# Performance work log

Measured on AMD Instinct MI355X. Metric: run time of the kernel, lower is better.

The kernel has to match this reference:

```python
import jax, jax.numpy as jnp
import numpy as np

B, N = 32, 512
N_DIM, N_P, N_K = 128, 3, 2
F0_DIM = N_DIM * N_P            # 384
CAT_DIM = N_DIM * (N_K + 1) * N_P  # 1152


def setup_inputs() -> dict:
    key = jax.random.key(0)
    ks = jax.random.split(key, 12)
    s = 0.05
    return {
        "loc": jax.random.uniform(ks[0], (B, N, 2), dtype=jnp.float32),
        "deadline": jax.random.uniform(ks[1], (B, N), dtype=jnp.float32),
        "workload": jax.random.uniform(ks[2], (B, N), dtype=jnp.float32),
        "depot": jax.random.uniform(ks[3], (B, 1, 2), dtype=jnp.float32),
        "W_init": jax.random.normal(ks[4], (3, F0_DIM), dtype=jnp.float32) * s,
        "b_init": jnp.zeros((F0_DIM,), jnp.float32),
        "W_dep": jax.random.normal(ks[5], (2, N_DIM), dtype=jnp.float32) * s,
        "b_dep": jnp.zeros((N_DIM,), jnp.float32),
        "W_g1": jax.random.normal(ks[6], (CAT_DIM, N_DIM), dtype=jnp.float32) * s,
        "b_g1": jnp.zeros((N_DIM,), jnp.float32),
        "W_g2": jax.random.normal(ks[7], (CAT_DIM, N_DIM), dtype=jnp.float32) * s,
        "b_g2": jnp.zeros((N_DIM,), jnp.float32),
        "W_g3": jax.random.normal(ks[8], (CAT_DIM, N_DIM), dtype=jnp.float32) * s,
        "b_g3": jnp.zeros((N_DIM,), jnp.float32),
        "gamma": jnp.ones((F0_DIM,), jnp.float32),
        "beta": jnp.zeros((F0_DIM,), jnp.float32),
        "W_F": jax.random.normal(ks[9], (F0_DIM, N_DIM), dtype=jnp.float32) * s,
        "b_F": jnp.zeros((N_DIM,), jnp.float32),
    }


def _forward(loc, deadline, workload, depot, W_init, b_init, W_dep, b_dep,
             W_g1, b_g1, W_g2, b_g2, W_g3, b_g3, gamma, beta, W_F, b_F):
    # X = [loc, deadline/deadline.max()] -> [B,N,3] (workload is concatenated then dropped in original)
    X = jnp.concatenate([loc, (deadline / deadline.max())[..., None]], axis=-1)
    n = X.shape[1]
    # pairwise squared distances [B,N,N]
    d2 = ((X[:, :, None, :] - X[:, None, :, :]) ** 2).sum(-1)
    off = ~jnp.eye(n, dtype=bool)                      # off-diagonal mask
    d2_safe = jnp.where(off, d2, 1.0)
    A = jnp.where(off, 1.0 / jnp.sqrt(d2_safe), 0.0)   # A = 1/dist off-diag, 0 on diag
    A = jnp.where(jnp.isnan(A), 0.0, A)                # A[A!=A]=0
    A = A / A.max()                                    # global max-normalize
    deg = A.sum(-1) - 1.0                              # (A.sum(-1) - 1)
    L = jnp.eye(n, dtype=A.dtype) * deg[:, None, :] - A  # D - A (diag = deg)
    L2 = L @ L

    F0 = X @ W_init + b_init                           # [B,N,384]
    F0_sq = F0 * F0
    F0_cu = F0 * F0_sq

    def prop(F):
        return jnp.concatenate([F, L @ F, L2 @ F], axis=-1)  # [B,N,1152]

    g1 = prop(F0) @ W_g1 + b_g1
    g2 = prop(F0_sq) @ W_g2 + b_g2
    g3 = prop(F0_cu) @ W_g3 + b_g3
    F1 = jnp.concatenate([g1, g2, g3], axis=-1)        # [B,N,384]
    F1 = jax.nn.leaky_relu(F1) + F0

    # BatchNorm1d (training mode): stats over flattened (B*N) samples, biased var
    flat = F1.reshape(-1, F1.shape[-1])
    mu = flat.mean(0)
    var = ((flat - mu) ** 2).mean(0)
    F1 = (F1 - mu) / jnp.sqrt(var + 1e-5) * gamma + beta

    F_final = jax.nn.leaky_relu(F1 @ W_F + b_F)        # [B,N,128]
    dep = depot @ W_dep + b_dep                        # [B,1,128]
    h = jnp.concatenate([dep, F_final], axis=1)        # [B,N+1,128]
    return h, h.mean(axis=1)


def reference(loc, deadline, workload, depot, W_init, b_init, W_dep, b_dep,
              W_g1, b_g1, W_g2, b_g2, W_g3, b_g3, gamma, beta, W_F, b_F):
    return _forward(loc, deadline, workload, depot, W_init, b_init, W_dep, b_dep,
                    W_g1, b_g1, W_g2, b_g2, W_g3, b_g3, gamma, beta, W_F, b_F)
```

## Files before the change

kernel.cpp:

```cpp
#include <hip/hip_runtime.h>

#define LEAKY(x) ((x) > 0.0f ? (x) : 0.01f * (x))

typedef __attribute__((ext_vector_type(8))) short bf16x8;
typedef __attribute__((ext_vector_type(4))) float f32x4;
typedef __attribute__((ext_vector_type(8))) unsigned short u16x8;
typedef __attribute__((ext_vector_type(4))) unsigned short u16x4;

__device__ __forceinline__ unsigned short f2bf(float f) {
    unsigned int u = __float_as_uint(f);
    unsigned int r = (u + 0x7fffu + ((u >> 16) & 1u)) >> 16;
    return (unsigned short)r;
}
__device__ __forceinline__ float bf2f(unsigned short u) {
    return __uint_as_float(((unsigned int)u) << 16);
}

__device__ __forceinline__ void lds_barrier() {
    __builtin_amdgcn_s_waitcnt(0xC07F);
    __builtin_amdgcn_s_barrier();
}


__global__ void k_dmax(const float* __restrict__ deadline, float* __restrict__ dmax) {
    __shared__ float red[256];
    int t = threadIdx.x;
    float m = -1e30f;
    for (int i = t; i < 16384; i += 256) m = fmaxf(m, deadline[i]);
    red[t] = m; __syncthreads();
    for (int s = 128; s > 0; s >>= 1) {
        if (t < s) red[t] = fmaxf(red[t], red[t + s]);
        __syncthreads();
    }
    if (t == 0) *dmax = red[0];
}

__global__ __launch_bounds__(256) void k_rowstats(const float* __restrict__ loc,
                                                  const float* __restrict__ deadline,
                                                  const float* __restrict__ dmaxv,
                                                  float* __restrict__ rowsum, float* __restrict__ pmax) {
    int blk = blockIdx.x;
    int wave = threadIdx.x >> 6, lane = threadIdx.x & 63;
    int bi = blk * 4 + wave;
    int b = bi >> 9, i = bi & 511;
    float invd = 1.0f / (*dmaxv);
    const float* lb = loc + b * 1024;
    const float* db = deadline + b * 512;
    float xi = lb[i * 2], yi = lb[i * 2 + 1], zi = db[i] * invd;
    float lsum = 0.f, lmax = 0.f;
    for (int j = lane; j < 512; j += 64) {
        float d0 = xi - lb[j * 2], d1 = yi - lb[j * 2 + 1], d2 = zi - db[j] * invd;
        float dd = d0 * d0 + d1 * d1 + d2 * d2;
        float r = (j == i) ? 0.f : rsqrtf(dd);
        lsum += r; lmax = fmaxf(lmax, r);
    }
    for (int off = 32; off > 0; off >>= 1) {
        lsum += __shfl_down(lsum, off);
        lmax = fmaxf(lmax, __shfl_down(lmax, off));
    }
    __shared__ float smax[4];
    if (lane == 0) { rowsum[bi] = lsum; smax[wave] = lmax; }
    __syncthreads();
    if (threadIdx.x == 0) pmax[blk] = fmaxf(fmaxf(smax[0], smax[1]), fmaxf(smax[2], smax[3]));
}

__global__ void k_amax(const float* __restrict__ pmax, float* __restrict__ amaxf) {
    __shared__ float red[256];
    int t = threadIdx.x;
    float m = 0.f;
    for (int i = t; i < 4096; i += 256) m = fmaxf(m, pmax[i]);
    red[t] = m; __syncthreads();
    for (int s = 128; s > 0; s >>= 1) {
        if (t < s) red[t] = fmaxf(red[t], red[t + s]);
        __syncthreads();
    }
    if (t == 0) *amaxf = red[0];
}

__global__ void k_buildL(const float* __restrict__ loc, const float* __restrict__ deadline,
                         const float* __restrict__ dmaxv, const float* __restrict__ rowsum,
                         const float* __restrict__ amaxf, unsigned short* __restrict__ Lb) {
    int id = blockIdx.x * 256 + threadIdx.x;
    float inv = 1.0f / (*amaxf);
    float invd = 1.0f / (*dmaxv);
    size_t e = (size_t)id * 4;
    size_t bi = e >> 9;
    int b = (int)(bi >> 9);
    int i = (int)(bi & 511);
    int j0 = (int)(e & 511);
    const float* lb = loc + b * 1024;
    const float* db = deadline + b * 512;
    float xi = lb[i * 2], yi = lb[i * 2 + 1], zi = db[i] * invd;
    float4 l01 = *(const float4*)(lb + j0 * 2);
    float4 l23 = *(const float4*)(lb + j0 * 2 + 4);
    float4 dj = *(const float4*)(db + j0);
    float diag = rowsum[bi] * inv - 1.0f;
    float jx[4] = {l01.x, l01.z, l23.x, l23.z};
    float jy[4] = {l01.y, l01.w, l23.y, l23.w};
    float jz[4] = {dj.x * invd, dj.y * invd, dj.z * invd, dj.w * invd};
    u16x4 o;
#pragma unroll
    for (int j = 0; j < 4; j++) {
        float d0 = xi - jx[j], d1 = yi - jy[j], d2 = zi - jz[j];
        float dd = d0 * d0 + d1 * d1 + d2 * d2;
        float v = (i == j0 + j) ? diag : -rsqrtf(dd) * inv;
        o[j] = f2bf(v);
    }
    *(u16x4*)(Lb + e) = o;
}

__global__ void k_F0powW(const float* __restrict__ loc, const float* __restrict__ deadline,
                         const float* __restrict__ dmaxv,
                         const float* __restrict__ Wi, const float* __restrict__ bi_,
                         const float* __restrict__ Wg1, const float* __restrict__ Wg2,
                         const float* __restrict__ Wg3,
                         unsigned short* __restrict__ P1, unsigned short* __restrict__ P2,
                         unsigned short* __restrict__ P3, unsigned short* __restrict__ WgT) {
    int bid = blockIdx.x;
    if (bid < 6144) {
        int id = bid * 256 + threadIdx.x;
        int row = id / 96, c4 = (id % 96) * 4;
        float x0 = loc[row * 2], x1 = loc[row * 2 + 1], x2 = deadline[row] / (*dmaxv);
        float4 w0 = *(const float4*)(Wi + c4);
        float4 w1 = *(const float4*)(Wi + 384 + c4);
        float4 w2 = *(const float4*)(Wi + 768 + c4);
        float4 bb = *(const float4*)(bi_ + c4);
        float f[4] = {x0 * w0.x + x1 * w1.x + x2 * w2.x + bb.x,
                      x0 * w0.y + x1 * w1.y + x2 * w2.y + bb.y,
                      x0 * w0.z + x1 * w1.z + x2 * w2.z + bb.z,
                      x0 * w0.w + x1 * w1.w + x2 * w2.w + bb.w};
        u16x4 o1, o2, o3;
#pragma unroll
        for (int j = 0; j < 4; j++) {
            o1[j] = f2bf(f[j]); o2[j] = f2bf(f[j] * f[j]); o3[j] = f2bf(f[j] * f[j] * f[j]);
        }
        size_t e = (size_t)row * 384 + c4;
        *(u16x4*)(P1 + e) = o1; *(u16x4*)(P2 + e) = o2; *(u16x4*)(P3 + e) = o3;
    } else {
        int id = (bid - 6144) * 256 + threadIdx.x;
        int combo = id / 49152, rem = id % 49152;
        int n = rem / 384, k = rem % 384;
        int kp = combo / 3, part = combo % 3;
        const float* W = (kp == 0) ? Wg1 : (kp == 1 ? Wg2 : Wg3);
        WgT[id] = f2bf(W[(part * 384 + k) * 128 + n]);
    }
}


__device__ __forceinline__ void pipe128x64(
    const unsigned short* __restrict__ A0, int As0, const unsigned short* __restrict__ B0, int Bs0, int it0,
    const unsigned short* __restrict__ A1, int As1, const unsigned short* __restrict__ B1, int Bs1, int it1,
    unsigned short* AsL, unsigned short* BsL,
    f32x4 (&acc)[4][2], int t)
{
    const int lane = t & 63, wave = t >> 6;
    const int wm = wave >> 1, wn = wave & 1;
    const int quad = lane >> 4, l16 = lane & 15;
    const int ra = t >> 1, ca = (t & 1) * 4;
    const int rb = t >> 2, cb = (t & 3) * 2;
    const unsigned short* Ar0 = A0 + (size_t)ra * As0;
    const unsigned short* Ar1 = A1 ? (A1 + (size_t)ra * As1) : Ar0;
    const unsigned short* Br0 = B0 + (size_t)rb * Bs0;
    const unsigned short* Br1 = B1 ? (B1 + (size_t)rb * Bs1) : Br0;
    const int total = it0 + it1;

    u16x8 paA[4], pbA[2], paB[4], pbB[2];
    auto loadStage = [&](int idx, u16x8 (&pa)[4], u16x8 (&pb)[2]) {
        int sg = (idx >= it0);
        int k0 = (sg ? idx - it0 : idx) * 64;
        const unsigned short* Ar = sg ? Ar1 : Ar0;
        const unsigned short* Br = sg ? Br1 : Br0;
#pragma unroll
        for (int j = 0; j < 4; j++) pa[j] = *(const u16x8*)(Ar + k0 + (ca + j) * 8);
#pragma unroll
        for (int j = 0; j < 2; j++) pb[j] = *(const u16x8*)(Br + k0 + (cb + j) * 8);
    };
    auto writeStage = [&](int bf_, u16x8 (&pa)[4], u16x8 (&pb)[2]) {
#pragma unroll
        for (int j = 0; j < 4; j++)
            *(u16x8*)(AsL + bf_ * 8192 + ra * 64 + (((ca + j) ^ (ra & 7)) * 8)) = pa[j];
#pragma unroll
        for (int j = 0; j < 2; j++)
            *(u16x8*)(BsL + bf_ * 4096 + rb * 64 + (((cb + j) ^ (rb & 7)) * 8)) = pb[j];
    };
    auto mfmaStep = [&](int bf_) {
#pragma unroll
        for (int h = 0; h < 2; h++) {
            bf16x8 af[4], bfr[2];
            int phys = ((h * 4 + quad) ^ (l16 & 7)) * 8;
#pragma unroll
            for (int i = 0; i < 4; i++)
                af[i] = *(const bf16x8*)(AsL + bf_ * 8192 + (wm * 64 + i * 16 + l16) * 64 + phys);
#pragma unroll
            for (int n = 0; n < 2; n++)
                bfr[n] = *(const bf16x8*)(BsL + bf_ * 4096 + (wn * 32 + n * 16 + l16) * 64 + phys);
#pragma unroll
            for (int i = 0; i < 4; i++)
#pragma unroll
                for (int n = 0; n < 2; n++)
                    acc[i][n] = __builtin_amdgcn_mfma_f32_16x16x32_bf16(af[i], bfr[n], acc[i][n], 0, 0, 0);
        }
    };

    loadStage(0, paA, pbA);
    loadStage(1, paB, pbB);
    int buf = 0;
    for (int s = 0; s < total; s += 2) {
        writeStage(buf, paA, pbA);
        lds_barrier();
        if (s + 2 < total) loadStage(s + 2, paA, pbA);
        mfmaStep(buf);
        buf ^= 1;
        writeStage(buf, paB, pbB);
        lds_barrier();
        if (s + 3 < total) loadStage(s + 3, paB, pbB);
        mfmaStep(buf);
        buf ^= 1;
    }
}

__device__ __forceinline__ void pipe64x64(
    const unsigned short* __restrict__ A0, int As0, const unsigned short* __restrict__ B0, int Bs0, int it0,
    unsigned short* AsL, unsigned short* BsL,
    f32x4 (&acc)[2][2], int t)
{
    const int lane = t & 63, wave = t >> 6;
    const int wm = wave >> 1, wn = wave & 1;
    const int quad = lane >> 4, l16 = lane & 15;
    const int rb = t >> 2, cb = (t & 3) * 2;
    const unsigned short* Ar0 = A0 + (size_t)rb * As0;
    const unsigned short* Br0 = B0 + (size_t)rb * Bs0;

    u16x8 paA[2], pbA[2], paB[2], pbB[2];
    auto loadStage = [&](int idx, u16x8 (&pa)[2], u16x8 (&pb)[2]) {
        int k0 = idx * 64;
#pragma unroll
        for (int j = 0; j < 2; j++) { pa[j] = *(const u16x8*)(Ar0 + k0 + (cb + j) * 8);
                                      pb[j] = *(const u16x8*)(Br0 + k0 + (cb + j) * 8); }
    };
    auto writeStage = [&](int bf_, u16x8 (&pa)[2], u16x8 (&pb)[2]) {
#pragma unroll
        for (int j = 0; j < 2; j++) {
            int phys = ((cb + j) ^ (rb & 7)) * 8;
            *(u16x8*)(AsL + bf_ * 4096 + rb * 64 + phys) = pa[j];
            *(u16x8*)(BsL + bf_ * 4096 + rb * 64 + phys) = pb[j];
        }
    };
    auto mfmaStep = [&](int bf_) {
#pragma unroll
        for (int h = 0; h < 2; h++) {
            bf16x8 af[2], bfr[2];
            int phys = ((h * 4 + quad) ^ (l16 & 7)) * 8;
#pragma unroll
            for (int i = 0; i < 2; i++)
                af[i] = *(const bf16x8*)(AsL + bf_ * 4096 + (wm * 32 + i * 16 + l16) * 64 + phys);
#pragma unroll
            for (int n = 0; n < 2; n++)
                bfr[n] = *(const bf16x8*)(BsL + bf_ * 4096 + (wn * 32 + n * 16 + l16) * 64 + phys);
#pragma unroll
            for (int i = 0; i < 2; i++)
#pragma unroll
                for (int n = 0; n < 2; n++)
                    acc[i][n] = __builtin_amdgcn_mfma_f32_16x16x32_bf16(af[i], bfr[n], acc[i][n], 0, 0, 0);
        }
    };

    loadStage(0, paA, pbA);
    loadStage(1, paB, pbB);
    int buf = 0;
    for (int s = 0; s < it0; s += 2) {
        writeStage(buf, paA, pbA);
        lds_barrier();
        if (s + 2 < it0) loadStage(s + 2, paA, pbA);
        mfmaStep(buf);
        buf ^= 1;
        writeStage(buf, paB, pbB);
        lds_barrier();
        if (s + 3 < it0) loadStage(s + 3, paB, pbB);
        mfmaStep(buf);
        buf ^= 1;
    }
}

__device__ __forceinline__ void storeCT_bf16(
    f32x4 (&acc)[4][2], unsigned short* LDSu, int t, unsigned short* __restrict__ dst)
{
    const int wave = t >> 6, lane = t & 63;
    const int wm = wave >> 1, wn = wave & 1;
    const int quad = lane >> 4, l16 = lane & 15;
    __syncthreads();
    unsigned short* Cs = LDSu;
#pragma unroll
    for (int i = 0; i < 4; i++)
#pragma unroll
        for (int n = 0; n < 2; n++)
#pragma unroll
            for (int r = 0; r < 4; r++)
                Cs[(wm * 64 + i * 16 + quad * 4 + r) * 72 + wn * 32 + n * 16 + l16] = f2bf(acc[i][n][r]);
    __syncthreads();
#pragma unroll
    for (int v = 0; v < 4; v++) {
        int chunk = t + v * 256;
        int row = chunk >> 3, c8 = (chunk & 7) * 8;
        u16x8 val = *(u16x8*)(Cs + row * 72 + c8);
        *(u16x8*)(dst + (size_t)row * 512 + c8) = val;
    }
}

__global__ __launch_bounds__(256) void k_ygemmT(
    const unsigned short* __restrict__ WgT,
    const unsigned short* __restrict__ P1, const unsigned short* __restrict__ P2,
    const unsigned short* __restrict__ P3, unsigned short* __restrict__ Y2T)
{
    __shared__ unsigned short LDSu[24576];
    const int t = threadIdx.x;
    const int id = blockIdx.x;
    const int b = id & 31, tt = id >> 5;
    const int kp = tt % 3, nb = tt / 3;
    const unsigned short* P = (kp == 0) ? P1 : (kp == 1 ? P2 : P3);
    f32x4 acc[4][2];
#pragma unroll
    for (int i = 0; i < 4; i++)
#pragma unroll
        for (int n = 0; n < 2; n++) acc[i][n] = (f32x4){0.f, 0.f, 0.f, 0.f};
    pipe128x64(WgT + (size_t)(kp * 3 + 2) * 49152, 384,
               P + ((size_t)b * 512 + nb * 64) * 384, 384, 6,
               nullptr, 0, nullptr, 0, 0, LDSu, LDSu + 16384, acc, t);
    storeCT_bf16(acc, LDSu, t, Y2T + ((size_t)b * 384 + kp * 128) * 512 + nb * 64);
}

__global__ __launch_bounds__(256) void k_lg1T(
    const unsigned short* __restrict__ Lb, const unsigned short* __restrict__ Y2T,
    const unsigned short* __restrict__ WgT,
    const unsigned short* __restrict__ P1, const unsigned short* __restrict__ P2,
    const unsigned short* __restrict__ P3, unsigned short* __restrict__ ZT)
{
    __shared__ unsigned short LDSu[24576];
    const int t = threadIdx.x;
    const int id = blockIdx.x;
    const int b = id & 31, tt = id >> 5;
    const int kp = tt % 3, nb = tt / 3;
    const unsigned short* P = (kp == 0) ? P1 : (kp == 1 ? P2 : P3);
    f32x4 acc[4][2];
#pragma unroll
    for (int i = 0; i < 4; i++)
#pragma unroll
        for (int n = 0; n < 2; n++) acc[i][n] = (f32x4){0.f, 0.f, 0.f, 0.f};
    pipe128x64(Y2T + (size_t)b * 196608 + (size_t)kp * 128 * 512, 512,
               Lb + (size_t)b * 262144 + (size_t)nb * 64 * 512, 512, 8,
               WgT + (size_t)(kp * 3 + 1) * 49152, 384,
               P + ((size_t)b * 512 + nb * 64) * 384, 384, 6, LDSu, LDSu + 16384, acc, t);
    storeCT_bf16(acc, LDSu, t, ZT + ((size_t)b * 384 + kp * 128) * 512 + nb * 64);
}

__global__ __launch_bounds__(256) void k_lg2(
    const unsigned short* __restrict__ Lb, const unsigned short* __restrict__ ZT,
    const unsigned short* __restrict__ WgT,
    const unsigned short* __restrict__ P1, const unsigned short* __restrict__ P2,
    const unsigned short* __restrict__ P3,
    const float* __restrict__ bg1, const float* __restrict__ bg2, const float* __restrict__ bg3,
    unsigned short* __restrict__ F1b, float* __restrict__ bn1, float* __restrict__ bn2)
{
    __shared__ unsigned short LDSu[24576];
    __shared__ float bnS[64], bnQ[64];
    const int t = threadIdx.x;
    const int id = blockIdx.x;
    const int b = id & 31, tt = id >> 5;
    const int gt = tt % 6, mb = tt / 6;
    const int kp = gt >> 1;
    if (t < 64) { bnS[t] = 0.f; bnQ[t] = 0.f; }
    const unsigned short* P = (kp == 0) ? P1 : (kp == 1 ? P2 : P3);
    f32x4 acc[4][2];
#pragma unroll
    for (int i = 0; i < 4; i++)
#pragma unroll
        for (int n = 0; n < 2; n++) acc[i][n] = (f32x4){0.f, 0.f, 0.f, 0.f};
    pipe128x64(Lb + (size_t)b * 262144 + (size_t)mb * 128 * 512, 512,
               ZT + (size_t)b * 196608 + (size_t)gt * 64 * 512, 512, 8,
               P + ((size_t)b * 512 + mb * 128) * 384, 384,
               WgT + (size_t)(kp * 3) * 49152 + (size_t)(gt & 1) * 64 * 384, 384, 6,
               LDSu, LDSu + 16384, acc, t);

    const int wave = t >> 6, lane = t & 63;
    const int wm = wave >> 1, wn = wave & 1;
    const int quad = lane >> 4, l16 = lane & 15;
    __syncthreads();
    float* Cf = (float*)LDSu;
#pragma unroll
    for (int i = 0; i < 4; i++)
#pragma unroll
        for (int n = 0; n < 2; n++)
#pragma unroll
            for (int r = 0; r < 4; r++)
                Cf[(wm * 64 + i * 16 + quad * 4 + r) * 68 + wn * 32 + n * 16 + l16] = acc[i][n][r];
    __syncthreads();

    const float* bg = (kp == 0) ? bg1 : (kp == 1 ? bg2 : bg3);
    float4 bgv = *(const float4*)(bg + (gt & 1) * 64 + (t & 15) * 4);
    float ls1[4] = {0.f, 0.f, 0.f, 0.f}, ls2[4] = {0.f, 0.f, 0.f, 0.f};
#pragma unroll
    for (int v = 0; v < 8; v++) {
        int chunk = t + v * 256;
        int row = chunk >> 4;
        int c4 = (chunk & 15) * 4;
        float4 a = *(float4*)(Cf + row * 68 + c4);
        size_t idx = ((size_t)b * 512 + mb * 128 + row) * 384 + gt * 64 + c4;
        u16x4 p = *(const u16x4*)(P1 + idx);
        float av[4] = {a.x, a.y, a.z, a.w};
        float bv[4] = {bgv.x, bgv.y, bgv.z, bgv.w};
        u16x4 o;
#pragma unroll
        for (int j = 0; j < 4; j++) {
            float c = av[j] + bv[j];
            float vv = LEAKY(c) + bf2f(p[j]);
            o[j] = f2bf(vv);
            ls1[j] += vv; ls2[j] += vv * vv;
        }
        *(u16x4*)(F1b + idx) = o;
    }
#pragma unroll
    for (int j = 0; j < 4; j++) {
        atomicAdd(&bnS[(t & 15) * 4 + j], ls1[j]);
        atomicAdd(&bnQ[(t & 15) * 4 + j], ls2[j]);
    }
    __syncthreads();
    if (t < 64) {
        atomicAdd(&bn1[gt * 64 + t], bnS[t]);
        atomicAdd(&bn2[gt * 64 + t], bnQ[t]);
    }
}

__global__ __launch_bounds__(384) void k_bnprep(
    const float* __restrict__ bn1, const float* __restrict__ bn2,
    const float* __restrict__ gamma, const float* __restrict__ beta,
    const float* __restrict__ WF, const float* __restrict__ bF,
    float* __restrict__ sS, float* __restrict__ beffv)
{
    __shared__ float ttL[384];
    int c = threadIdx.x;
    float mu = bn1[c] * (1.f / 16384.f);
    float var = bn2[c] * (1.f / 16384.f) - mu * mu;
    float sc = gamma[c] / sqrtf(var + 1e-5f);
    sS[c] = sc;
    ttL[c] = beta[c] - mu * sc;
    __syncthreads();
    if (c < 128) {
        float a = bF[c];
        for (int k = 0; k < 384; k++) a += ttL[k] * WF[k * 128 + c];
        beffv[c] = a;
    }
}

__global__ void k_foldDep(const float* __restrict__ WF, const float* __restrict__ sS,
                          const float* __restrict__ depot, const float* __restrict__ Wd,
                          const float* __restrict__ bd,
                          unsigned short* __restrict__ WFsT, float* __restrict__ out) {
    int bid = blockIdx.x, t = threadIdx.x;
    if (bid < 192) {
        int id = bid * 256 + t;
        int n = id / 384, k = id % 384;
        WFsT[id] = f2bf(WF[k * 128 + n] * sS[k]);
    } else {
        int id = (bid - 192) * 256 + t;
        int b = id >> 7, o = id & 127;
        out[(size_t)b * 65664 + o] = depot[b * 2] * Wd[o] + depot[b * 2 + 1] * Wd[128 + o] + bd[o];
    }
}

__global__ __launch_bounds__(256) void k_fgemm(
    const unsigned short* __restrict__ F1b, const unsigned short* __restrict__ WFsT,
    const float* __restrict__ beffv, float* __restrict__ out, float* __restrict__ msum)
{
    __shared__ unsigned short LDSu[16384];
    __shared__ float msS[64];
    const int t = threadIdx.x;
    const int id = blockIdx.x;
    const int b = id & 31, tt = id >> 5;
    const int seg = tt >> 1, nt = tt & 1;
    if (t < 64) msS[t] = 0.f;
    f32x4 acc[2][2];
#pragma unroll
    for (int i = 0; i < 2; i++)
#pragma unroll
        for (int n = 0; n < 2; n++) acc[i][n] = (f32x4){0.f, 0.f, 0.f, 0.f};
    pipe64x64(F1b + ((size_t)b * 512 + seg * 64) * 384, 384,
              WFsT + (size_t)nt * 64 * 384, 384, 6, LDSu, LDSu + 8192, acc, t);

    const int wave = t >> 6, lane = t & 63;
    const int wm = wave >> 1, wn = wave & 1;
    const int quad = lane >> 4, l16 = lane & 15;
    __syncthreads();
    float* Cf = (float*)LDSu;
#pragma unroll
    for (int i = 0; i < 2; i++)
#pragma unroll
        for (int n = 0; n < 2; n++)
#pragma unroll
            for (int r = 0; r < 4; r++)
                Cf[(wm * 32 + i * 16 + quad * 4 + r) * 68 + wn * 32 + n * 16 + l16] = acc[i][n][r];
    __syncthreads();

    float4 be = *(const float4*)(beffv + nt * 64 + (t & 15) * 4);
    float ls[4] = {0.f, 0.f, 0.f, 0.f};
#pragma unroll
    for (int v = 0; v < 4; v++) {
        int chunk = t + v * 256;
        int row = chunk >> 4;
        int c4 = (chunk & 15) * 4;
        float4 a = *(float4*)(Cf + row * 68 + c4);
        float av[4] = {a.x, a.y, a.z, a.w};
        float bv[4] = {be.x, be.y, be.z, be.w};
        float vv0 = LEAKY(av[0] + bv[0]); ls[0] += vv0;
        float vv1 = LEAKY(av[1] + bv[1]); ls[1] += vv1;
        float vv2 = LEAKY(av[2] + bv[2]); ls[2] += vv2;
        float vv3 = LEAKY(av[3] + bv[3]); ls[3] += vv3;
        *(float4*)(out + (size_t)b * 65664 + (size_t)(seg * 64 + row + 1) * 128 + nt * 64 + c4)
            = make_float4(vv0, vv1, vv2, vv3);
    }
#pragma unroll
    for (int j = 0; j < 4; j++) atomicAdd(&msS[(t & 15) * 4 + j], ls[j]);
    __syncthreads();
    if (t < 64) atomicAdd(&msum[b * 128 + nt * 64 + t], msS[t]);
}

__global__ void k_mean(const float* __restrict__ msum, float* __restrict__ out) {
    int id = blockIdx.x * 256 + threadIdx.x;
    int b = id >> 7, o = id & 127;
    float dep = out[(size_t)b * 65664 + o];
    out[2101248 + id] = (msum[id] + dep) * (1.0f / 513.0f);
}


extern "C" void kernel_launch(void* const* d_in, const int* in_sizes, int n_in,
                              void* d_out, int out_size, void* d_ws, size_t ws_size,
                              hipStream_t stream) {
    const float* loc      = (const float*)d_in[0];
    const float* deadline = (const float*)d_in[1];
    const float* depot    = (const float*)d_in[3];
    const float* W_init   = (const float*)d_in[4];
    const float* b_init   = (const float*)d_in[5];
    const float* W_dep    = (const float*)d_in[6];
    const float* b_dep    = (const float*)d_in[7];
    const float* W_g1     = (const float*)d_in[8];
    const float* b_g1     = (const float*)d_in[9];
    const float* W_g2     = (const float*)d_in[10];
    const float* b_g2     = (const float*)d_in[11];
    const float* W_g3     = (const float*)d_in[12];
    const float* b_g3     = (const float*)d_in[13];
    const float* gamma    = (const float*)d_in[14];
    const float* beta     = (const float*)d_in[15];
    const float* W_F      = (const float*)d_in[16];
    const float* b_F      = (const float*)d_in[17];
    float* out = (float*)d_out;
    float* ws  = (float*)d_ws;

    float* dmaxv  = ws + 0;
    float* amaxf  = ws + 4;
    float* bn1    = ws + 8;
    float* bn2    = ws + 392;
    float* msum   = ws + 776;
    float* rowsum = ws + 4872;
    float* pmax   = ws + 21256;
    float* sS     = ws + 25352;
    float* beffv  = ws + 25736;
    unsigned short* Lb   = (unsigned short*)(ws + 25864);
    unsigned short* P1   = (unsigned short*)(ws + 4220168);
    unsigned short* P2   = (unsigned short*)(ws + 7365896);
    unsigned short* P3   = (unsigned short*)(ws + 10511624);
    unsigned short* WgT  = (unsigned short*)(ws + 13657352);
    unsigned short* WFsT = (unsigned short*)(ws + 13878536);
    unsigned short* Y2T  = (unsigned short*)(ws + 13903112);
    unsigned short* ZT   = (unsigned short*)(ws + 17048840);
    unsigned short* F1b  = (unsigned short*)(ws + 20194568);

    hipMemsetAsync(bn1, 0, (384 + 384 + 4096) * sizeof(float), stream);

    k_dmax<<<1, 256, 0, stream>>>(deadline, dmaxv);
    k_rowstats<<<4096, 256, 0, stream>>>(loc, deadline, dmaxv, rowsum, pmax);
    k_amax<<<1, 256, 0, stream>>>(pmax, amaxf);
    k_buildL<<<8192, 256, 0, stream>>>(loc, deadline, dmaxv, rowsum, amaxf, Lb);
    k_F0powW<<<7872, 256, 0, stream>>>(loc, deadline, dmaxv, W_init, b_init,
                                       W_g1, W_g2, W_g3, P1, P2, P3, WgT);

    k_ygemmT<<<768, 256, 0, stream>>>(WgT, P1, P2, P3, Y2T);
    k_lg1T<<<768, 256, 0, stream>>>(Lb, Y2T, WgT, P1, P2, P3, ZT);
    k_lg2<<<768, 256, 0, stream>>>(Lb, ZT, WgT, P1, P2, P3,
                                   b_g1, b_g2, b_g3, F1b, bn1, bn2);

    k_bnprep<<<1, 384, 0, stream>>>(bn1, bn2, gamma, beta, W_F, b_F, sS, beffv);
    k_foldDep<<<208, 256, 0, stream>>>(W_F, sS, depot, W_dep, b_dep, WFsT, out);
    k_fgemm<<<512, 256, 0, stream>>>(F1b, WFsT, beffv, out, msum);
    k_mean<<<16, 256, 0, stream>>>(msum, out);
}
```

Measured before the change: 241.2 us.

## Use 128x128 output tiles for L-propagation GEMMs and regroup block-to-batch mapping

The two Laplacian propagation GEMMs (k_lg1T, k_lg2) switch from 128x64 tiles with K-step 64 to 128x128 tiles with K-step 32, halving their grid to 384 blocks. This doubles per-block data reuse and cuts redundant loads of L and the weight/feature operands. All GEMM kernels also remap block IDs so that eight consecutive blocks cover eight batches of the same tile, which may change L2 locality. The k_lg2 epilogue now applies bias and leaky ReLU before staging results to LDS as bf16, adding an extra rounding step. The larger tile raises accumulator register use and leaves fewer blocks to fill the CUs.

Result: slower. 250.6 us (+3.9%).

```diff
diff --git a/kernel.cpp b/kernel.cpp
--- a/kernel.cpp
+++ b/kernel.cpp
@@ -149,7 +149,6 @@
 
 __device__ __forceinline__ void pipe128x64(
     const unsigned short* __restrict__ A0, int As0, const unsigned short* __restrict__ B0, int Bs0, int it0,
-    const unsigned short* __restrict__ A1, int As1, const unsigned short* __restrict__ B1, int Bs1, int it1,
     unsigned short* AsL, unsigned short* BsL,
     f32x4 (&acc)[4][2], int t)
 {
@@ -159,21 +158,15 @@
     const int ra = t >> 1, ca = (t & 1) * 4;
     const int rb = t >> 2, cb = (t & 3) * 2;
     const unsigned short* Ar0 = A0 + (size_t)ra * As0;
-    const unsigned short* Ar1 = A1 ? (A1 + (size_t)ra * As1) : Ar0;
     const unsigned short* Br0 = B0 + (size_t)rb * Bs0;
-    const unsigned short* Br1 = B1 ? (B1 + (size_t)rb * Bs1) : Br0;
-    const int total = it0 + it1;
 
     u16x8 paA[4], pbA[2], paB[4], pbB[2];
     auto loadStage = [&](int idx, u16x8 (&pa)[4], u16x8 (&pb)[2]) {
-        int sg = (idx >= it0);
-        int k0 = (sg ? idx - it0 : idx) * 64;
-        const unsigned short* Ar = sg ? Ar1 : Ar0;
-        const unsigned short* Br = sg ? Br1 : Br0;
-#pragma unroll
-        for (int j = 0; j < 4; j++) pa[j] = *(const u16x8*)(Ar + k0 + (ca + j) * 8);
-#pragma unroll
-        for (int j = 0; j < 2; j++) pb[j] = *(const u16x8*)(Br + k0 + (cb + j) * 8);
+        int k0 = idx * 64;
+#pragma unroll
+        for (int j = 0; j < 4; j++) pa[j] = *(const u16x8*)(Ar0 + k0 + (ca + j) * 8);
+#pragma unroll
+        for (int j = 0; j < 2; j++) pb[j] = *(const u16x8*)(Br0 + k0 + (cb + j) * 8);
     };
     auto writeStage = [&](int bf_, u16x8 (&pa)[4], u16x8 (&pb)[2]) {
 #pragma unroll
@@ -196,69 +189,6 @@
                 bfr[n] = *(const bf16x8*)(BsL + bf_ * 4096 + (wn * 32 + n * 16 + l16) * 64 + phys);
 #pragma unroll
             for (int i = 0; i < 4; i++)
-#pragma unroll
-                for (int n = 0; n < 2; n++)
-                    acc[i][n] = __builtin_amdgcn_mfma_f32_16x16x32_bf16(af[i], bfr[n], acc[i][n], 0, 0, 0);
-        }
-    };
-
-    loadStage(0, paA, pbA);
-    loadStage(1, paB, pbB);
-    int buf = 0;
-    for (int s = 0; s < total; s += 2) {
-        writeStage(buf, paA, pbA);
-        lds_barrier();
-        if (s + 2 < total) loadStage(s + 2, paA, pbA);
-        mfmaStep(buf);
-        buf ^= 1;
-        writeStage(buf, paB, pbB);
-        lds_barrier();
-        if (s + 3 < total) loadStage(s + 3, paB, pbB);
-        mfmaStep(buf);
-        buf ^= 1;
-    }
-}
-
-__device__ __forceinline__ void pipe64x64(
-    const unsigned short* __restrict__ A0, int As0, const unsigned short* __restrict__ B0, int Bs0, int it0,
-    unsigned short* AsL, unsigned short* BsL,
-    f32x4 (&acc)[2][2], int t)
-{
-    const int lane = t & 63, wave = t >> 6;
-    const int wm = wave >> 1, wn = wave & 1;
-    const int quad = lane >> 4, l16 = lane & 15;
-    const int rb = t >> 2, cb = (t & 3) * 2;
-    const unsigned short* Ar0 = A0 + (size_t)rb * As0;
-    const unsigned short* Br0 = B0 + (size_t)rb * Bs0;
-
-    u16x8 paA[2], pbA[2], paB[2], pbB[2];
-    auto loadStage = [&](int idx, u16x8 (&pa)[2], u16x8 (&pb)[2]) {
-        int k0 = idx * 64;
-#pragma unroll
-        for (int j = 0; j < 2; j++) { pa[j] = *(const u16x8*)(Ar0 + k0 + (cb + j) * 8);
-                                      pb[j] = *(const u16x8*)(Br0 + k0 + (cb + j) * 8); }
-    };
-    auto writeStage = [&](int bf_, u16x8 (&pa)[2], u16x8 (&pb)[2]) {
-#pragma unroll
-        for (int j = 0; j < 2; j++) {
-            int phys = ((cb + j) ^ (rb & 7)) * 8;
-            *(u16x8*)(AsL + bf_ * 4096 + rb * 64 + phys) = pa[j];
-            *(u16x8*)(BsL + bf_ * 4096 + rb * 64 + phys) = pb[j];
-        }
-    };
-    auto mfmaStep = [&](int bf_) {
-#pragma unroll
-        for (int h = 0; h < 2; h++) {
-            bf16x8 af[2], bfr[2];
-            int phys = ((h * 4 + quad) ^ (l16 & 7)) * 8;
-#pragma unroll
-            for (int i = 0; i < 2; i++)
-                af[i] = *(const bf16x8*)(AsL + bf_ * 4096 + (wm * 32 + i * 16 + l16) * 64 + phys);
-#pragma unroll
-            for (int n = 0; n < 2; n++)
-                bfr[n] = *(const bf16x8*)(BsL + bf_ * 4096 + (wn * 32 + n * 16 + l16) * 64 + phys);
-#pragma unroll
-            for (int i = 0; i < 2; i++)
 #pragma unroll
                 for (int n = 0; n < 2; n++)
                     acc[i][n] = __builtin_amdgcn_mfma_f32_16x16x32_bf16(af[i], bfr[n], acc[i][n], 0, 0, 0);
@@ -282,6 +212,136 @@
     }
 }
 
+__device__ __forceinline__ void pipe128x128(
+    const unsigned short* __restrict__ A0, int As0, const unsigned short* __restrict__ B0, int Bs0, int it0,
+    const unsigned short* __restrict__ A1, int As1, const unsigned short* __restrict__ B1, int Bs1, int it1,
+    unsigned short* AsL, unsigned short* BsL,
+    f32x4 (&acc)[4][4], int t)
+{
+    const int lane = t & 63, wave = t >> 6;
+    const int wm = wave >> 1, wn = wave & 1;
+    const int quad = lane >> 4, l16 = lane & 15;
+    const int r_ = t >> 1, c_ = (t & 1) * 2;
+    const unsigned short* ArA = A0 + (size_t)r_ * As0;
+    const unsigned short* ArB = A1 ? (A1 + (size_t)r_ * As1) : ArA;
+    const unsigned short* BrA = B0 + (size_t)r_ * Bs0;
+    const unsigned short* BrB = B1 ? (B1 + (size_t)r_ * Bs1) : BrA;
+    const int total = it0 + it1;
+
+    u16x8 pa0[2], pb0[2], pa1[2], pb1[2];
+    auto loadStage = [&](int idx, u16x8 (&pa)[2], u16x8 (&pb)[2]) {
+        int sg = (idx >= it0);
+        int k0 = (sg ? idx - it0 : idx) * 32;
+        const unsigned short* Ar = sg ? ArB : ArA;
+        const unsigned short* Br = sg ? BrB : BrA;
+#pragma unroll
+        for (int j = 0; j < 2; j++) { pa[j] = *(const u16x8*)(Ar + k0 + (c_ + j) * 8);
+                                      pb[j] = *(const u16x8*)(Br + k0 + (c_ + j) * 8); }
+    };
+    auto writeStage = [&](int bf_, u16x8 (&pa)[2], u16x8 (&pb)[2]) {
+#pragma unroll
+        for (int j = 0; j < 2; j++) {
+            int phys = ((c_ + j) ^ (r_ & 3)) * 8;
+            *(u16x8*)(AsL + bf_ * 4096 + r_ * 32 + phys) = pa[j];
+            *(u16x8*)(BsL + bf_ * 4096 + r_ * 32 + phys) = pb[j];
+        }
+    };
+    auto mfmaStep = [&](int bf_) {
+        bf16x8 af[4], bfr[4];
+        int phys = (quad ^ (l16 & 3)) * 8;
+#pragma unroll
+        for (int i = 0; i < 4; i++)
+            af[i] = *(const bf16x8*)(AsL + bf_ * 4096 + (wm * 64 + i * 16 + l16) * 32 + phys);
+#pragma unroll
+        for (int n = 0; n < 4; n++)
+            bfr[n] = *(const bf16x8*)(BsL + bf_ * 4096 + (wn * 64 + n * 16 + l16) * 32 + phys);
+#pragma unroll
+        for (int i = 0; i < 4; i++)
+#pragma unroll
+            for (int n = 0; n < 4; n++)
+                acc[i][n] = __builtin_amdgcn_mfma_f32_16x16x32_bf16(af[i], bfr[n], acc[i][n], 0, 0, 0);
+    };
+
+    loadStage(0, pa0, pb0);
+    loadStage(1, pa1, pb1);
+    int buf = 0;
+    for (int s = 0; s < total; s += 2) {
+        writeStage(buf, pa0, pb0);
+        lds_barrier();
+        if (s + 2 < total) loadStage(s + 2, pa0, pb0);
+        mfmaStep(buf);
+        buf ^= 1;
+        writeStage(buf, pa1, pb1);
+        lds_barrier();
+        if (s + 3 < total) loadStage(s + 3, pa1, pb1);
+        mfmaStep(buf);
+        buf ^= 1;
+    }
+}
+
+__device__ __forceinline__ void pipe64x64(
+    const unsigned short* __restrict__ A0, int As0, const unsigned short* __restrict__ B0, int Bs0, int it0,
+    unsigned short* AsL, unsigned short* BsL,
+    f32x4 (&acc)[2][2], int t)
+{
+    const int lane = t & 63, wave = t >> 6;
+    const int wm = wave >> 1, wn = wave & 1;
+    const int quad = lane >> 4, l16 = lane & 15;
+    const int rb = t >> 2, cb = (t & 3) * 2;
+    const unsigned short* Ar0 = A0 + (size_t)rb * As0;
+    const unsigned short* Br0 = B0 + (size_t)rb * Bs0;
+
+    u16x8 paA[2], pbA[2], paB[2], pbB[2];
+    auto loadStage = [&](int idx, u16x8 (&pa)[2], u16x8 (&pb)[2]) {
+        int k0 = idx * 64;
+#pragma unroll
+        for (int j = 0; j < 2; j++) { pa[j] = *(const u16x8*)(Ar0 + k0 + (cb + j) * 8);
+                                      pb[j] = *(const u16x8*)(Br0 + k0 + (cb + j) * 8); }
+    };
+    auto writeStage = [&](int bf_, u16x8 (&pa)[2], u16x8 (&pb)[2]) {
+#pragma unroll
+        for (int j = 0; j < 2; j++) {
+            int phys = ((cb + j) ^ (rb & 7)) * 8;
+            *(u16x8*)(AsL + bf_ * 4096 + rb * 64 + phys) = pa[j];
+            *(u16x8*)(BsL + bf_ * 4096 + rb * 64 + phys) = pb[j];
+        }
+    };
+    auto mfmaStep = [&](int bf_) {
+#pragma unroll
+        for (int h = 0; h < 2; h++) {
+            bf16x8 af[2], bfr[2];
+            int phys = ((h * 4 + quad) ^ (l16 & 7)) * 8;
+#pragma unroll
+            for (int i = 0; i < 2; i++)
+                af[i] = *(const bf16x8*)(AsL + bf_ * 4096 + (wm * 32 + i * 16 + l16) * 64 + phys);
+#pragma unroll
+            for (int n = 0; n < 2; n++)
+                bfr[n] = *(const bf16x8*)(BsL + bf_ * 4096 + (wn * 32 + n * 16 + l16) * 64 + phys);
+#pragma unroll
+            for (int i = 0; i < 2; i++)
+#pragma unroll
+                for (int n = 0; n < 2; n++)
+                    acc[i][n] = __builtin_amdgcn_mfma_f32_16x16x32_bf16(af[i], bfr[n], acc[i][n], 0, 0, 0);
+        }
+    };
+
+    loadStage(0, paA, pbA);
+    loadStage(1, paB, pbB);
+    int buf = 0;
+    for (int s = 0; s < it0; s += 2) {
+        writeStage(buf, paA, pbA);
+        lds_barrier();
+        if (s + 2 < it0) loadStage(s + 2, paA, pbA);
+        mfmaStep(buf);
+        buf ^= 1;
+        writeStage(buf, paB, pbB);
+        lds_barrier();
+        if (s + 3 < it0) loadStage(s + 3, paB, pbB);
+        mfmaStep(buf);
+        buf ^= 1;
+    }
+}
+
 __device__ __forceinline__ void storeCT_bf16(
     f32x4 (&acc)[4][2], unsigned short* LDSu, int t, unsigned short* __restrict__ dst)
 {
@@ -289,21 +349,42 @@
     const int wm = wave >> 1, wn = wave & 1;
     const int quad = lane >> 4, l16 = lane & 15;
     __syncthreads();
-    unsigned short* Cs = LDSu;
 #pragma unroll
     for (int i = 0; i < 4; i++)
 #pragma unroll
         for (int n = 0; n < 2; n++)
 #pragma unroll
             for (int r = 0; r < 4; r++)
-                Cs[(wm * 64 + i * 16 + quad * 4 + r) * 72 + wn * 32 + n * 16 + l16] = f2bf(acc[i][n][r]);
+                LDSu[(wm * 64 + i * 16 + quad * 4 + r) * 72 + wn * 32 + n * 16 + l16] = f2bf(acc[i][n][r]);
     __syncthreads();
 #pragma unroll
     for (int v = 0; v < 4; v++) {
         int chunk = t + v * 256;
         int row = chunk >> 3, c8 = (chunk & 7) * 8;
-        u16x8 val = *(u16x8*)(Cs + row * 72 + c8);
-        *(u16x8*)(dst + (size_t)row * 512 + c8) = val;
+        *(u16x8*)(dst + (size_t)row * 512 + c8) = *(u16x8*)(LDSu + row * 72 + c8);
+    }
+}
+
+__device__ __forceinline__ void storeCT128(
+    f32x4 (&acc)[4][4], unsigned short* LDSu, int t, unsigned short* __restrict__ dst)
+{
+    const int wave = t >> 6, lane = t & 63;
+    const int wm = wave >> 1, wn = wave & 1;
+    const int quad = lane >> 4, l16 = lane & 15;
+    __syncthreads();
+#pragma unroll
+    for (int i = 0; i < 4; i++)
+#pragma unroll
+        for (int n = 0; n < 4; n++)
+#pragma unroll
+            for (int r = 0; r < 4; r++)
+                LDSu[(wm * 64 + i * 16 + quad * 4 + r) * 136 + wn * 64 + n * 16 + l16] = f2bf(acc[i][n][r]);
+    __syncthreads();
+#pragma unroll
+    for (int v = 0; v < 8; v++) {
+        int chunk = t + v * 256;
+        int row = chunk >> 4, c8 = (chunk & 15) * 8;
+        *(u16x8*)(dst + (size_t)row * 512 + c8) = *(u16x8*)(LDSu + row * 136 + c8);
     }
 }
 
@@ -315,8 +396,10 @@
     __shared__ unsigned short LDSu[24576];
     const int t = threadIdx.x;
     const int id = blockIdx.x;
-    const int b = id & 31, tt = id >> 5;
-    const int kp = tt % 3, nb = tt / 3;
+    const int hi = id >> 3;
+    const int tile = hi % 24;
+    const int b = (id & 7) + ((hi / 24) << 3);
+    const int kp = tile % 3, nb = tile / 3;
     const unsigned short* P = (kp == 0) ? P1 : (kp == 1 ? P2 : P3);
     f32x4 acc[4][2];
 #pragma unroll
@@ -325,7 +408,7 @@
         for (int n = 0; n < 2; n++) acc[i][n] = (f32x4){0.f, 0.f, 0.f, 0.f};
     pipe128x64(WgT + (size_t)(kp * 3 + 2) * 49152, 384,
                P + ((size_t)b * 512 + nb * 64) * 384, 384, 6,
-               nullptr, 0, nullptr, 0, 0, LDSu, LDSu + 16384, acc, t);
+               LDSu, LDSu + 16384, acc, t);
     storeCT_bf16(acc, LDSu, t, Y2T + ((size_t)b * 384 + kp * 128) * 512 + nb * 64);
 }
 
@@ -335,22 +418,25 @@
     const unsigned short* __restrict__ P1, const unsigned short* __restrict__ P2,
     const unsigned short* __restrict__ P3, unsigned short* __restrict__ ZT)
 {
-    __shared__ unsigned short LDSu[24576];
+    __shared__ unsigned short LDSu[17408];
     const int t = threadIdx.x;
     const int id = blockIdx.x;
-    const int b = id & 31, tt = id >> 5;
-    const int kp = tt % 3, nb = tt / 3;
+    const int hi = id >> 3;
+    const int tile = hi % 12;
+    const int b = (id & 7) + ((hi / 12) << 3);
+    const int kp = tile % 3, nb = tile / 3;
     const unsigned short* P = (kp == 0) ? P1 : (kp == 1 ? P2 : P3);
-    f32x4 acc[4][2];
+    f32x4 acc[4][4];
 #pragma unroll
     for (int i = 0; i < 4; i++)
 #pragma unroll
-        for (int n = 0; n < 2; n++) acc[i][n] = (f32x4){0.f, 0.f, 0.f, 0.f};
-    pipe128x64(Y2T + (size_t)b * 196608 + (size_t)kp * 128 * 512, 512,
-               Lb + (size_t)b * 262144 + (size_t)nb * 64 * 512, 512, 8,
-               WgT + (size_t)(kp * 3 + 1) * 49152, 384,
-               P + ((size_t)b * 512 + nb * 64) * 384, 384, 6, LDSu, LDSu + 16384, acc, t);
-    storeCT_bf16(acc, LDSu, t, ZT + ((size_t)b * 384 + kp * 128) * 512 + nb * 64);
+        for (int n = 0; n < 4; n++) acc[i][n] = (f32x4){0.f, 0.f, 0.f, 0.f};
+    pipe128x128(Y2T + (size_t)b * 196608 + (size_t)kp * 128 * 512, 512,
+                Lb + (size_t)b * 262144 + (size_t)nb * 128 * 512, 512, 16,
+                WgT + (size_t)(kp * 3 + 1) * 49152, 384,
+                P + ((size_t)b * 512 + nb * 128) * 384, 384, 12,
+                LDSu, LDSu + 8192, acc, t);
+    storeCT128(acc, LDSu, t, ZT + ((size_t)b * 384 + kp * 128) * 512 + nb * 128);
 }
 
 __global__ __launch_bounds__(256) void k_lg2(
@@ -361,72 +447,73 @@
     const float* __restrict__ bg1, const float* __restrict__ bg2, const float* __restrict__ bg3,
     unsigned short* __restrict__ F1b, float* __restrict__ bn1, float* __restrict__ bn2)
 {
-    __shared__ unsigned short LDSu[24576];
-    __shared__ float bnS[64], bnQ[64];
+    __shared__ unsigned short LDSu[17408];
+    __shared__ float bnS[128], bnQ[128];
     const int t = threadIdx.x;
     const int id = blockIdx.x;
-    const int b = id & 31, tt = id >> 5;
-    const int gt = tt % 6, mb = tt / 6;
-    const int kp = gt >> 1;
-    if (t < 64) { bnS[t] = 0.f; bnQ[t] = 0.f; }
-    const unsigned short* P = (kp == 0) ? P1 : (kp == 1 ? P2 : P3);
-    f32x4 acc[4][2];
+    const int hi = id >> 3;
+    const int tile = hi % 12;
+    const int b = (id & 7) + ((hi / 12) << 3);
+    const int mb = tile & 3, gt = tile >> 2;
+    if (t < 128) { bnS[t] = 0.f; bnQ[t] = 0.f; }
+    const unsigned short* P = (gt == 0) ? P1 : (gt == 1 ? P2 : P3);
+    f32x4 acc[4][4];
 #pragma unroll
     for (int i = 0; i < 4; i++)
 #pragma unroll
-        for (int n = 0; n < 2; n++) acc[i][n] = (f32x4){0.f, 0.f, 0.f, 0.f};
-    pipe128x64(Lb + (size_t)b * 262144 + (size_t)mb * 128 * 512, 512,
-               ZT + (size_t)b * 196608 + (size_t)gt * 64 * 512, 512, 8,
-               P + ((size_t)b * 512 + mb * 128) * 384, 384,
-               WgT + (size_t)(kp * 3) * 49152 + (size_t)(gt & 1) * 64 * 384, 384, 6,
-               LDSu, LDSu + 16384, acc, t);
+        for (int n = 0; n < 4; n++) acc[i][n] = (f32x4){0.f, 0.f, 0.f, 0.f};
+    pipe128x128(Lb + (size_t)b * 262144 + (size_t)mb * 128 * 512, 512,
+                ZT + (size_t)b * 196608 + (size_t)gt * 128 * 512, 512, 16,
+                P + ((size_t)b * 512 + mb * 128) * 384, 384,
+                WgT + (size_t)(gt * 3) * 49152, 384, 12,
+                LDSu, LDSu + 8192, acc, t);
 
     const int wave = t >> 6, lane = t & 63;
     const int wm = wave >> 1, wn = wave & 1;
     const int quad = lane >> 4, l16 = lane & 15;
-    __syncthreads();
-    float* Cf = (float*)LDSu;
+    const float* bg = (gt == 0) ? bg1 : (gt == 1 ? bg2 : bg3);
+    __syncthreads();
 #pragma unroll
     for (int i = 0; i < 4; i++)
 #pragma unroll
-        for (int n = 0; n < 2; n++)
-#pragma unroll
-            for (int r = 0; r < 4; r++)
-                Cf[(wm * 64 + i * 16 + quad * 4 + r) * 68 + wn * 32 + n * 16 + l16] = acc[i][n][r];
-    __syncthreads();
-
-    const float* bg = (kp == 0) ? bg1 : (kp == 1 ? bg2 : bg3);
-    float4 bgv = *(const float4*)(bg + (gt & 1) * 64 + (t & 15) * 4);
-    float ls1[4] = {0.f, 0.f, 0.f, 0.f}, ls2[4] = {0.f, 0.f, 0.f, 0.f};
+        for (int n = 0; n < 4; n++) {
+            int colL = wn * 64 + n * 16 + l16;
+            float bias = bg[colL];
+#pragma unroll
+            for (int r = 0; r < 4; r++) {
+                float c = acc[i][n][r] + bias;
+                LDSu[(wm * 64 + i * 16 + quad * 4 + r) * 136 + colL] = f2bf(LEAKY(c));
+            }
+        }
+    __syncthreads();
+    float ls1[8] = {0.f,0.f,0.f,0.f,0.f,0.f,0.f,0.f};
+    float ls2[8] = {0.f,0.f,0.f,0.f,0.f,0.f,0.f,0.f};
 #pragma unroll
     for (int v = 0; v < 8; v++) {
         int chunk = t + v * 256;
         int row = chunk >> 4;
-        int c4 = (chunk & 15) * 4;
-        float4 a = *(float4*)(Cf + row * 68 + c4);
-        size_t idx = ((size_t)b * 512 + mb * 128 + row) * 384 + gt * 64 + c4;
-        u16x4 p = *(const u16x4*)(P1 + idx);
-        float av[4] = {a.x, a.y, a.z, a.w};
-        float bv[4] = {bgv.x, bgv.y, bgv.z, bgv.w};
-        u16x4 o;
-#pragma unroll
-        for (int j = 0; j < 4; j++) {
-            float c = av[j] + bv[j];
-            float vv = LEAKY(c) + bf2f(p[j]);
+        int c8 = (chunk & 15) * 8;
+        size_t idx = ((size_t)b * 512 + mb * 128 + row) * 384 + gt * 128 + c8;
+        u16x8 st = *(u16x8*)(LDSu + row * 136 + c8);
+        u16x8 p  = *(const u16x8*)(P1 + idx);
+        u16x8 o;
+#pragma unroll
+        for (int j = 0; j < 8; j++) {
+            float vv = bf2f(st[j]) + bf2f(p[j]);
             o[j] = f2bf(vv);
             ls1[j] += vv; ls2[j] += vv * vv;
         }
-        *(u16x4*)(F1b + idx) = o;
-    }
-#pragma unroll
-    for (int j = 0; j < 4; j++) {
-        atomicAdd(&bnS[(t & 15) * 4 + j], ls1[j]);
-        atomicAdd(&bnQ[(t & 15) * 4 + j], ls2[j]);
-    }
-    __syncthreads();
-    if (t < 64) {
-        atomicAdd(&bn1[gt * 64 + t], bnS[t]);
-        atomicAdd(&bn2[gt * 64 + t], bnQ[t]);
+        *(u16x8*)(F1b + idx) = o;
+    }
+#pragma unroll
+    for (int j = 0; j < 8; j++) {
+        atomicAdd(&bnS[(t & 15) * 8 + j], ls1[j]);
+        atomicAdd(&bnQ[(t & 15) * 8 + j], ls2[j]);
+    }
+    __syncthreads();
+    if (t < 128) {
+        atomicAdd(&bn1[gt * 128 + t], bnS[t]);
+        atomicAdd(&bn2[gt * 128 + t], bnQ[t]);
     }
 }
 
@@ -475,8 +562,10 @@
     __shared__ float msS[64];
     const int t = threadIdx.x;
     const int id = blockIdx.x;
-    const int b = id & 31, tt = id >> 5;
-    const int seg = tt >> 1, nt = tt & 1;
+    const int hi = id >> 3;
+    const int tile = hi % 16;
+    const int b = (id & 7) + ((hi / 16) << 3);
+    const int seg = tile >> 1, nt = tile & 1;
     if (t < 64) msS[t] = 0.f;
     f32x4 acc[2][2];
 #pragma unroll
@@ -508,12 +597,10 @@
         int row = chunk >> 4;
         int c4 = (chunk & 15) * 4;
         float4 a = *(float4*)(Cf + row * 68 + c4);
-        float av[4] = {a.x, a.y, a.z, a.w};
-        float bv[4] = {be.x, be.y, be.z, be.w};
-        float vv0 = LEAKY(av[0] + bv[0]); ls[0] += vv0;
-        float vv1 = LEAKY(av[1] + bv[1]); ls[1] += vv1;
-        float vv2 = LEAKY(av[2] + bv[2]); ls[2] += vv2;
-        float vv3 = LEAKY(av[3] + bv[3]); ls[3] += vv3;
+        float vv0 = LEAKY(a.x + be.x); ls[0] += vv0;
+        float vv1 = LEAKY(a.y + be.y); ls[1] += vv1;
+        float vv2 = LEAKY(a.z + be.z); ls[2] += vv2;
+        float vv3 = LEAKY(a.w + be.w); ls[3] += vv3;
         *(float4*)(out + (size_t)b * 65664 + (size_t)(seg * 64 + row + 1) * 128 + nt * 64 + c4)
             = make_float4(vv0, vv1, vv2, vv3);
     }
@@ -583,8 +670,8 @@
                                        W_g1, W_g2, W_g3, P1, P2, P3, WgT);
 
     k_ygemmT<<<768, 256, 0, stream>>>(WgT, P1, P2, P3, Y2T);
-    k_lg1T<<<768, 256, 0, stream>>>(Lb, Y2T, WgT, P1, P2, P3, ZT);
-    k_lg2<<<768, 256, 0, stream>>>(Lb, ZT, WgT, P1, P2, P3,
+    k_lg1T<<<384, 256, 0, stream>>>(Lb, Y2T, WgT, P1, P2, P3, ZT);
+    k_lg2<<<384, 256, 0, stream>>>(Lb, ZT, WgT, P1, P2, P3,
                                    b_g1, b_g2, b_g3, F1b, bn1, bn2);
 
     k_bnprep<<<1, 384, 0, stream>>>(bn1, bn2, gamma, beta, W_F, b_F, sS, beffv);
```
